# Optimization experiments

Measured on AMD Instinct MI355X. Metric: run time of the kernel, lower is better.

The kernel has to match this reference:

```python
import jax, jax.numpy as jnp
import numpy as np

N = 100000   # nodes
F = 128      # input features
H = 128      # hidden = 2*output_dim
Z = 64       # output_dim
E = 1600000  # message-passing edges
EP = 200000  # pos/neg decode edges each


def setup_inputs() -> dict:
    key = jax.random.key(0)
    ks = jax.random.split(key, 6)
    x = jax.random.normal(ks[0], (N, F), dtype=jnp.float32)
    edge_index = jax.random.randint(ks[1], (2, E), 0, N, dtype=jnp.int64)
    pos_edge = jax.random.randint(ks[2], (2, EP), 0, N, dtype=jnp.int64)
    neg_edge = jax.random.randint(ks[3], (2, EP), 0, N, dtype=jnp.int64)
    W1 = jax.random.normal(ks[4], (F, H), dtype=jnp.float32) / np.float32(np.sqrt(F))
    b1 = jnp.zeros((H,), jnp.float32)
    W2 = jax.random.normal(ks[5], (H, Z), dtype=jnp.float32) / np.float32(np.sqrt(H))
    b2 = jnp.zeros((Z,), jnp.float32)
    return dict(x=x, W1=W1, b1=b1, W2=W2, b2=b2,
                edge_index=edge_index, pos_edge=pos_edge, neg_edge=neg_edge)


def _gcn_conv(x, src, dst, norm, W, b, n):
    # x' = scatter_add_dst(norm * (x @ W)[src]) + b   (GCNConv, sym-normalized, self-loops)
    h = x @ W                         # [N, out]
    msg = h[src] * norm[:, None]      # [E+N, out] gather + scale
    out = jax.ops.segment_sum(msg, dst, num_segments=n)
    return out + b


def reference(x, W1, b1, W2, b2, edge_index, pos_edge, neg_edge):
    # add self-loops (GCNConv default)
    loop = jnp.arange(N, dtype=edge_index.dtype)
    src = jnp.concatenate([edge_index[0], loop])
    dst = jnp.concatenate([edge_index[1], loop])
    # symmetric normalization deg^-1/2[src] * deg^-1/2[dst]
    deg = jax.ops.segment_sum(jnp.ones(dst.shape, x.dtype), dst, num_segments=N)
    dinv = jnp.where(deg > 0, jax.lax.rsqrt(deg), 0.0)
    norm = dinv[src] * dinv[dst]
    # encoder: GCN -> ReLU -> GCN
    h = jax.nn.relu(_gcn_conv(x, src, dst, norm, W1, b1, N))
    latent = _gcn_conv(h, src, dst, norm, W2, b2, N)
    # decoder: edge dot products on pos+neg edges
    e = jnp.concatenate([pos_edge, neg_edge], axis=-1)  # [2, 2*EP]
    logits = jnp.sum(latent[e[0]] * latent[e[1]], axis=-1)
    return logits
```

## Files before the change

kernel.cpp:

```cpp
#include <hip/hip_runtime.h>

#define N_NODES 100000
#define F_IN    128
#define H_DIM   128
#define Z_DIM   64
#define E_EDGES 1600000
#define EP_EDGES 200000

#define BSHIFT 7
#define NBUCK  ((N_NODES + 127) >> 7)
#define CHUNK  4096
#define NCHUNK ((E_EDGES + CHUNK - 1) / CHUNK)

typedef __attribute__((ext_vector_type(8))) short short8;
typedef __attribute__((ext_vector_type(4))) float f32x4;
typedef unsigned int uint;
typedef unsigned short ushort;

__device__ __forceinline__ ushort f2bf(float f) {
    uint u = __float_as_uint(f);
    u += 0x7fffu + ((u >> 16) & 1u);
    return (ushort)(u >> 16);
}
__device__ __forceinline__ float bflo(uint u) { return __uint_as_float(u << 16); }
__device__ __forceinline__ float bfhi(uint u) { return __uint_as_float(u & 0xffff0000u); }


__global__ __launch_bounds__(256) void zero_gcur_kernel(int* __restrict__ gcur) {
    int i = blockIdx.x * 256 + threadIdx.x;
    if (i < 1024) gcur[i] = 0;
}


__global__ __launch_bounds__(256) void bhist_kernel(const int* __restrict__ dst,
                                                    int* __restrict__ ghist) {
    __shared__ int lh[NBUCK];
    for (int i = threadIdx.x; i < NBUCK; i += 256) lh[i] = 0;
    __syncthreads();
    int base = blockIdx.x * CHUNK;
    int end = min(base + CHUNK, E_EDGES);
    for (int e = base + threadIdx.x; e < end; e += 256)
        atomicAdd(&lh[dst[e] >> BSHIFT], 1);
    __syncthreads();
    for (int i = threadIdx.x; i < NBUCK; i += 256)
        if (lh[i]) atomicAdd(&ghist[i], lh[i]);
}


__global__ __launch_bounds__(1024) void bscan_kernel(int* __restrict__ gc) {
    __shared__ int s[1024];
    int t = threadIdx.x;
    int v = (t < NBUCK) ? gc[t] : 0;
    s[t] = v;
    __syncthreads();
    #pragma unroll
    for (int off = 1; off < 1024; off <<= 1) {
        int x = (t >= off) ? s[t - off] : 0;
        __syncthreads();
        s[t] += x;
        __syncthreads();
    }
    if (t < NBUCK) gc[t] = s[t] - v;
}


__global__ __launch_bounds__(256) void bscatter_kernel(const int* __restrict__ src,
                                                       const int* __restrict__ dst,
                                                       int* __restrict__ gcursor,
                                                       int* __restrict__ sorted) {
    __shared__ int lh[NBUCK];
    __shared__ int lbase[NBUCK];
    for (int i = threadIdx.x; i < NBUCK; i += 256) lh[i] = 0;
    __syncthreads();
    int base = blockIdx.x * CHUNK;
    int end = min(base + CHUNK, E_EDGES);
    for (int e = base + threadIdx.x; e < end; e += 256)
        atomicAdd(&lh[dst[e] >> BSHIFT], 1);
    __syncthreads();
    for (int i = threadIdx.x; i < NBUCK; i += 256)
        lbase[i] = lh[i] ? atomicAdd(&gcursor[i], lh[i]) : 0;
    __syncthreads();
    for (int e = base + threadIdx.x; e < end; e += 256) {
        int d = dst[e];
        int p = atomicAdd(&lbase[d >> BSHIFT], 1);
        sorted[p] = (src[e] << 7) | (d & 127);
    }
}


__global__ __launch_bounds__(256) void bucket_csr_kernel(const int* __restrict__ sorted,
                                                         const int* __restrict__ gcur,
                                                         int* __restrict__ csr,
                                                         int* __restrict__ ends,
                                                         float* __restrict__ dinv) {
    __shared__ int lcnt[128], lcur[128];
    int b = blockIdx.x, t = threadIdx.x;
    int bstart = b ? gcur[b - 1] : 0;
    int bend = gcur[b];
    if (t < 128) lcnt[t] = 0;
    __syncthreads();
    for (int i = bstart + t; i < bend; i += 256)
        atomicAdd(&lcnt[sorted[i] & 127], 1);
    __syncthreads();
    if (t < 64) {
        int c0 = lcnt[t], c1 = lcnt[t + 64];
        int s0 = c0;
        #pragma unroll
        for (int d = 1; d < 64; d <<= 1) {
            int x = __shfl_up(s0, d, 64);
            if (t >= d) s0 += x;
        }
        int tot0 = __shfl(s0, 63, 64);
        int s1 = c1;
        #pragma unroll
        for (int d = 1; d < 64; d <<= 1) {
            int x = __shfl_up(s1, d, 64);
            if (t >= d) s1 += x;
        }
        s1 += tot0;
        lcur[t] = s0 - c0;
        lcur[t + 64] = s1 - c1;
        int n0 = b * 128 + t, n1 = n0 + 64;
        if (n0 < N_NODES) { ends[n0] = bstart + s0; dinv[n0] = rsqrtf(1.0f + (float)c0); }
        if (n1 < N_NODES) { ends[n1] = bstart + s1; dinv[n1] = rsqrtf(1.0f + (float)c1); }
    }
    __syncthreads();
    for (int i = bstart + t; i < bend; i += 256) {
        int v = sorted[i];
        int p = bstart + atomicAdd(&lcur[v & 127], 1);
        csr[p] = v >> 7;
    }
}


__global__ __launch_bounds__(256) void wprep_kernel(const float* __restrict__ W1,
                                                    const float* __restrict__ W2,
                                                    ushort* __restrict__ W1T,
                                                    ushort* __restrict__ W2T) {
    int i = blockIdx.x * 256 + threadIdx.x;
    if (i < 128 * 128) {
        int n = i >> 7, k = i & 127;
        W1T[i] = f2bf(W1[k * 128 + n]);
    }
    int j = i - 128 * 128;
    if (j >= 0 && j < 64 * 128) {
        int n = j >> 7, k = j & 127;
        W2T[j] = f2bf(W2[k * 64 + n]);
    }
}


template<int NC, bool A_F32>
__global__ __launch_bounds__(256) void gemm_mfma_kernel(const void* __restrict__ Ap,
                                                        const ushort* __restrict__ BT,
                                                        const float* __restrict__ dinv,
                                                        ushort* __restrict__ C, int M) {
    constexpr int NT = NC / 16;
    __shared__ ushort Bs[4 * NT * 64 * 8];

    for (int idx = threadIdx.x; idx < 4 * NT * 64; idx += 256) {
        int l   = idx & 63;
        int nt  = (idx >> 6) % NT;
        int kc  = idx / (64 * NT);
        int m16 = l & 15, quad = l >> 4;
        ((short8*)Bs)[idx] =
            *(const short8*)(BT + ((nt * 16 + m16) * 128 + kc * 32 + quad * 8));
    }
    __syncthreads();

    int wave = threadIdx.x >> 6, lane = threadIdx.x & 63;
    int m16 = lane & 15, quad = lane >> 4;
    int row0 = (blockIdx.x * 4 + wave) * 16;
    if (row0 >= M) return;
    int arow = row0 + m16;
    if (arow >= M) arow = M - 1;

    f32x4 acc[NT];
    #pragma unroll
    for (int t = 0; t < NT; ++t) acc[t] = (f32x4){0.f, 0.f, 0.f, 0.f};

    #pragma unroll
    for (int kc = 0; kc < 4; ++kc) {
        short8 a;
        if (A_F32) {
            const float* A = (const float*)Ap;
            const float4* p = (const float4*)(A + (size_t)arow * 128 + kc * 32 + quad * 8);
            float4 x0 = p[0], x1 = p[1];
            a[0] = (short)f2bf(x0.x); a[1] = (short)f2bf(x0.y);
            a[2] = (short)f2bf(x0.z); a[3] = (short)f2bf(x0.w);
            a[4] = (short)f2bf(x1.x); a[5] = (short)f2bf(x1.y);
            a[6] = (short)f2bf(x1.z); a[7] = (short)f2bf(x1.w);
        } else {
            a = *(const short8*)((const ushort*)Ap + (size_t)arow * 128 + kc * 32 + quad * 8);
        }
        #pragma unroll
        for (int nt = 0; nt < NT; ++nt) {
            short8 b = ((const short8*)Bs)[(kc * NT + nt) * 64 + lane];
            acc[nt] = __builtin_amdgcn_mfma_f32_16x16x32_bf16(a, b, acc[nt], 0, 0, 0);
        }
    }

    #pragma unroll
    for (int r = 0; r < 4; ++r) {
        int row = row0 + quad * 4 + r;
        if (row < M) {
            float dr = dinv[row];
            #pragma unroll
            for (int nt = 0; nt < NT; ++nt)
                C[(size_t)row * NC + nt * 16 + m16] = f2bf(acc[nt][r] * dr);
        }
    }
}


__global__ __launch_bounds__(256) void gather128_kernel(const ushort* __restrict__ feat,
                                                        const float* __restrict__ bias,
                                                        const float* __restrict__ dinv,
                                                        const int* __restrict__ ends,
                                                        const int* __restrict__ csr,
                                                        ushort* __restrict__ out) {
    int wave = threadIdx.x >> 6, lane = threadIdx.x & 63;
    int half = lane >> 5, sl = lane & 31;
    int n = blockIdx.x * 4 + wave;
    const uint2* fu = (const uint2*)feat;

    float a0 = 0.f, a1 = 0.f, a2 = 0.f, a3 = 0.f;
    if (half == 0) {
        uint2 s = fu[(size_t)n * 32 + sl];
        a0 = bflo(s.x); a1 = bfhi(s.x); a2 = bflo(s.y); a3 = bfhi(s.y);
    }
    int j0 = n ? ends[n - 1] : 0, j1 = ends[n];
    int j = j0 + half;
    for (; j + 14 < j1; j += 16) {
        int s0 = csr[j],      s1 = csr[j + 2],  s2 = csr[j + 4],  s3 = csr[j + 6];
        int s4 = csr[j + 8],  s5 = csr[j + 10], s6 = csr[j + 12], s7 = csr[j + 14];
        uint2 f0 = fu[(size_t)s0 * 32 + sl];
        uint2 f1 = fu[(size_t)s1 * 32 + sl];
        uint2 f2 = fu[(size_t)s2 * 32 + sl];
        uint2 f3 = fu[(size_t)s3 * 32 + sl];
        uint2 f4 = fu[(size_t)s4 * 32 + sl];
        uint2 f5 = fu[(size_t)s5 * 32 + sl];
        uint2 f6 = fu[(size_t)s6 * 32 + sl];
        uint2 f7 = fu[(size_t)s7 * 32 + sl];
        a0 += bflo(f0.x) + bflo(f1.x) + bflo(f2.x) + bflo(f3.x)
            + bflo(f4.x) + bflo(f5.x) + bflo(f6.x) + bflo(f7.x);
        a1 += bfhi(f0.x) + bfhi(f1.x) + bfhi(f2.x) + bfhi(f3.x)
            + bfhi(f4.x) + bfhi(f5.x) + bfhi(f6.x) + bfhi(f7.x);
        a2 += bflo(f0.y) + bflo(f1.y) + bflo(f2.y) + bflo(f3.y)
            + bflo(f4.y) + bflo(f5.y) + bflo(f6.y) + bflo(f7.y);
        a3 += bfhi(f0.y) + bfhi(f1.y) + bfhi(f2.y) + bfhi(f3.y)
            + bfhi(f4.y) + bfhi(f5.y) + bfhi(f6.y) + bfhi(f7.y);
    }
    for (; j + 6 < j1; j += 8) {
        int s0 = csr[j], s1 = csr[j + 2], s2 = csr[j + 4], s3 = csr[j + 6];
        uint2 f0 = fu[(size_t)s0 * 32 + sl];
        uint2 f1 = fu[(size_t)s1 * 32 + sl];
        uint2 f2 = fu[(size_t)s2 * 32 + sl];
        uint2 f3 = fu[(size_t)s3 * 32 + sl];
        a0 += bflo(f0.x) + bflo(f1.x) + bflo(f2.x) + bflo(f3.x);
        a1 += bfhi(f0.x) + bfhi(f1.x) + bfhi(f2.x) + bfhi(f3.x);
        a2 += bflo(f0.y) + bflo(f1.y) + bflo(f2.y) + bflo(f3.y);
        a3 += bfhi(f0.y) + bfhi(f1.y) + bfhi(f2.y) + bfhi(f3.y);
    }
    for (; j < j1; j += 2) {
        uint2 f = fu[(size_t)csr[j] * 32 + sl];
        a0 += bflo(f.x); a1 += bfhi(f.x); a2 += bflo(f.y); a3 += bfhi(f.y);
    }
    a0 += __shfl_xor(a0, 32, 64);
    a1 += __shfl_xor(a1, 32, 64);
    a2 += __shfl_xor(a2, 32, 64);
    a3 += __shfl_xor(a3, 32, 64);
    if (half == 0) {
        float dn = dinv[n];
        float r0 = fmaxf(bias[sl * 4 + 0] + dn * a0, 0.f);
        float r1 = fmaxf(bias[sl * 4 + 1] + dn * a1, 0.f);
        float r2 = fmaxf(bias[sl * 4 + 2] + dn * a2, 0.f);
        float r3 = fmaxf(bias[sl * 4 + 3] + dn * a3, 0.f);
        uint2 o;
        o.x = (uint)f2bf(r0) | ((uint)f2bf(r1) << 16);
        o.y = (uint)f2bf(r2) | ((uint)f2bf(r3) << 16);
        ((uint2*)out)[(size_t)n * 32 + sl] = o;
    }
}


__global__ __launch_bounds__(256) void gather64_kernel(const ushort* __restrict__ feat,
                                                       const float* __restrict__ bias,
                                                       const float* __restrict__ dinv,
                                                       const int* __restrict__ ends,
                                                       const int* __restrict__ csr,
                                                       ushort* __restrict__ outB) {
    int wave = threadIdx.x >> 6, lane = threadIdx.x & 63;
    int half = lane >> 5, sl = lane & 31;
    int n = blockIdx.x * 4 + wave;
    const uint* fu = (const uint*)feat;

    float a0 = 0.f, a1 = 0.f;
    if (half == 0) {
        uint s = fu[(size_t)n * 32 + sl];
        a0 = bflo(s); a1 = bfhi(s);
    }
    int j0 = n ? ends[n - 1] : 0, j1 = ends[n];
    int j = j0 + half;
    for (; j + 14 < j1; j += 16) {
        int s0 = csr[j],      s1 = csr[j + 2],  s2 = csr[j + 4],  s3 = csr[j + 6];
        int s4 = csr[j + 8],  s5 = csr[j + 10], s6 = csr[j + 12], s7 = csr[j + 14];
        uint f0 = fu[(size_t)s0 * 32 + sl];
        uint f1 = fu[(size_t)s1 * 32 + sl];
        uint f2 = fu[(size_t)s2 * 32 + sl];
        uint f3 = fu[(size_t)s3 * 32 + sl];
        uint f4 = fu[(size_t)s4 * 32 + sl];
        uint f5 = fu[(size_t)s5 * 32 + sl];
        uint f6 = fu[(size_t)s6 * 32 + sl];
        uint f7 = fu[(size_t)s7 * 32 + sl];
        a0 += bflo(f0) + bflo(f1) + bflo(f2) + bflo(f3)
            + bflo(f4) + bflo(f5) + bflo(f6) + bflo(f7);
        a1 += bfhi(f0) + bfhi(f1) + bfhi(f2) + bfhi(f3)
            + bfhi(f4) + bfhi(f5) + bfhi(f6) + bfhi(f7);
    }
    for (; j + 6 < j1; j += 8) {
        int s0 = csr[j], s1 = csr[j + 2], s2 = csr[j + 4], s3 = csr[j + 6];
        uint f0 = fu[(size_t)s0 * 32 + sl];
        uint f1 = fu[(size_t)s1 * 32 + sl];
        uint f2 = fu[(size_t)s2 * 32 + sl];
        uint f3 = fu[(size_t)s3 * 32 + sl];
        a0 += bflo(f0) + bflo(f1) + bflo(f2) + bflo(f3);
        a1 += bfhi(f0) + bfhi(f1) + bfhi(f2) + bfhi(f3);
    }
    for (; j < j1; j += 2) {
        uint f = fu[(size_t)csr[j] * 32 + sl];
        a0 += bflo(f); a1 += bfhi(f);
    }
    a0 += __shfl_xor(a0, 32, 64);
    a1 += __shfl_xor(a1, 32, 64);
    if (half == 0) {
        float dn = dinv[n];
        float o0 = bias[sl * 2]     + dn * a0;
        float o1 = bias[sl * 2 + 1] + dn * a1;
        ((uint*)outB)[(size_t)n * 32 + sl] = (uint)f2bf(o0) | ((uint)f2bf(o1) << 16);
    }
}


__global__ __launch_bounds__(256) void decode_kernel(const ushort* __restrict__ latentB,
                                                     const int* __restrict__ pos,
                                                     const int* __restrict__ neg,
                                                     float* __restrict__ out) {
    int gwave = (blockIdx.x * 256 + threadIdx.x) >> 6;
    int lane = threadIdx.x & 63;
    int half = lane >> 5, sl = lane & 31;
    const uint* L = (const uint*)latentB;
    int e0 = gwave * 8 + half * 4;
    if (e0 >= 2 * EP_EDGES) return;

    int ia[4], ib[4];
    #pragma unroll
    for (int u = 0; u < 4; ++u) {
        int edge = e0 + u;
        if (edge < EP_EDGES) {
            ia[u] = pos[edge];
            ib[u] = pos[EP_EDGES + edge];
        } else {
            int e2 = edge - EP_EDGES;
            ia[u] = neg[e2];
            ib[u] = neg[EP_EDGES + e2];
        }
    }
    uint la[4], lb[4];
    #pragma unroll
    for (int u = 0; u < 4; ++u) {
        la[u] = L[(size_t)ia[u] * 32 + sl];
        lb[u] = L[(size_t)ib[u] * 32 + sl];
    }
    float v[4];
    #pragma unroll
    for (int u = 0; u < 4; ++u)
        v[u] = bflo(la[u]) * bflo(lb[u]) + bfhi(la[u]) * bfhi(lb[u]);
    #pragma unroll
    for (int u = 0; u < 4; ++u) {
        float s = v[u];
        #pragma unroll
        for (int off = 16; off > 0; off >>= 1) s += __shfl_down(s, off, 64);
        if (sl == 0) out[e0 + u] = s;
    }
}


extern "C" void kernel_launch(void* const* d_in, const int* in_sizes, int n_in,
                              void* d_out, int out_size, void* d_ws, size_t ws_size,
                              hipStream_t stream) {
    const float* x  = (const float*)d_in[0];
    const float* W1 = (const float*)d_in[1];
    const float* b1 = (const float*)d_in[2];
    const float* W2 = (const float*)d_in[3];
    const float* b2 = (const float*)d_in[4];
    const int* edge_index = (const int*)d_in[5];
    const int* pos = (const int*)d_in[6];
    const int* neg = (const int*)d_in[7];
    float* out = (float*)d_out;

    const int* src = edge_index;
    const int* dst = edge_index + E_EDGES;

    float*  dinv   = (float*)d_ws;
    int*    ends   = (int*)(dinv + N_NODES);
    int*    gcur   = ends + N_NODES;
    int*    sorted = gcur + 1024;
    int*    csr    = sorted + E_EDGES;
    ushort* W1T    = (ushort*)(csr + E_EDGES);
    ushort* W2T    = W1T + 128 * 128;
    ushort* bufH   = W2T + 64 * 128;
    ushort* bufR   = bufH + (size_t)N_NODES * 128;

    zero_gcur_kernel<<<4, 256, 0, stream>>>(gcur);
    bhist_kernel<<<NCHUNK, 256, 0, stream>>>(dst, gcur);
    bscan_kernel<<<1, 1024, 0, stream>>>(gcur);
    bscatter_kernel<<<NCHUNK, 256, 0, stream>>>(src, dst, gcur, sorted);
    bucket_csr_kernel<<<NBUCK, 256, 0, stream>>>(sorted, gcur, csr, ends, dinv);

    wprep_kernel<<<96, 256, 0, stream>>>(W1, W2, W1T, W2T);

    const int GEMM_GRID = (N_NODES + 63) / 64;

    gemm_mfma_kernel<128, true><<<GEMM_GRID, 256, 0, stream>>>(x, W1T, dinv, bufH, N_NODES);

    gather128_kernel<<<N_NODES / 4, 256, 0, stream>>>(bufH, b1, dinv, ends, csr, bufR);

    gemm_mfma_kernel<64, false><<<GEMM_GRID, 256, 0, stream>>>(bufR, W2T, dinv, bufH, N_NODES);

    ushort* latentB = bufR;
    gather64_kernel<<<N_NODES / 4, 256, 0, stream>>>(bufH, b2, dinv, ends, csr, latentB);

    decode_kernel<<<(2 * EP_EDGES) / 32, 256, 0, stream>>>(latentB, pos, neg, out);
}
```

Before: 322.6 us.

## Replace scatter-time global atomics with per-chunk offset table and per-wave local counts

The histogram kernel now writes each chunk's per-bucket counts to a table, and a new column-wise scan kernel turns those counts into deterministic per-chunk base offsets. The scatter pass then no longer recomputes the local histogram or does global atomics. It only loads its precomputed bases. The CSR build splits its LDS counters per wave to reduce atomic contention, and the weight-prep kernel is merged with zeroing the counters to save a launch. In exchange it adds an extra scan kernel and a table of NCHUNK×NBUCK ints read and written through global memory.

```diff
diff --git a/kernel.cpp b/kernel.cpp
--- a/kernel.cpp
+++ b/kernel.cpp
@@ -26,14 +26,28 @@
 __device__ __forceinline__ float bfhi(uint u) { return __uint_as_float(u & 0xffff0000u); }
 
 
-__global__ __launch_bounds__(256) void zero_gcur_kernel(int* __restrict__ gcur) {
+__global__ __launch_bounds__(256) void wprep_kernel(const float* __restrict__ W1,
+                                                    const float* __restrict__ W2,
+                                                    ushort* __restrict__ W1T,
+                                                    ushort* __restrict__ W2T,
+                                                    int* __restrict__ gcur) {
     int i = blockIdx.x * 256 + threadIdx.x;
     if (i < 1024) gcur[i] = 0;
+    if (i < 128 * 128) {
+        int n = i >> 7, k = i & 127;
+        W1T[i] = f2bf(W1[k * 128 + n]);
+    }
+    int j = i - 128 * 128;
+    if (j >= 0 && j < 64 * 128) {
+        int n = j >> 7, k = j & 127;
+        W2T[j] = f2bf(W2[k * 64 + n]);
+    }
 }
 
 
 __global__ __launch_bounds__(256) void bhist_kernel(const int* __restrict__ dst,
-                                                    int* __restrict__ ghist) {
+                                                    int* __restrict__ gcur,
+                                                    int* __restrict__ tbl) {
     __shared__ int lh[NBUCK];
     for (int i = threadIdx.x; i < NBUCK; i += 256) lh[i] = 0;
     __syncthreads();
@@ -42,8 +56,12 @@
     for (int e = base + threadIdx.x; e < end; e += 256)
         atomicAdd(&lh[dst[e] >> BSHIFT], 1);
     __syncthreads();
-    for (int i = threadIdx.x; i < NBUCK; i += 256)
-        if (lh[i]) atomicAdd(&ghist[i], lh[i]);
+    int* trow = tbl + (size_t)blockIdx.x * NBUCK;
+    for (int i = threadIdx.x; i < NBUCK; i += 256) {
+        int c = lh[i];
+        trow[i] = c;
+        if (c) atomicAdd(&gcur[i], c);
+    }
 }
 
 
@@ -64,22 +82,36 @@
 }
 
 
+__global__ __launch_bounds__(512) void chunk_scan_kernel(int* __restrict__ tbl,
+                                                         const int* __restrict__ gcur) {
+    __shared__ int s[512];
+    int b = blockIdx.x, t = threadIdx.x;
+    int v = (t < NCHUNK) ? tbl[(size_t)t * NBUCK + b] : 0;
+    s[t] = v;
+    __syncthreads();
+    #pragma unroll
+    for (int off = 1; off < 512; off <<= 1) {
+        int x = (t >= off) ? s[t - off] : 0;
+        __syncthreads();
+        s[t] += x;
+        __syncthreads();
+    }
+    if (t < NCHUNK)
+        tbl[(size_t)t * NBUCK + b] = gcur[b] + (s[t] - v);
+}
+
+
 __global__ __launch_bounds__(256) void bscatter_kernel(const int* __restrict__ src,
                                                        const int* __restrict__ dst,
-                                                       int* __restrict__ gcursor,
+                                                       const int* __restrict__ tbl,
                                                        int* __restrict__ sorted) {
-    __shared__ int lh[NBUCK];
     __shared__ int lbase[NBUCK];
-    for (int i = threadIdx.x; i < NBUCK; i += 256) lh[i] = 0;
-    __syncthreads();
-    int base = blockIdx.x * CHUNK;
+    int c = blockIdx.x;
+    const int* trow = tbl + (size_t)c * NBUCK;
+    for (int i = threadIdx.x; i < NBUCK; i += 256) lbase[i] = trow[i];
+    __syncthreads();
+    int base = c * CHUNK;
     int end = min(base + CHUNK, E_EDGES);
-    for (int e = base + threadIdx.x; e < end; e += 256)
-        atomicAdd(&lh[dst[e] >> BSHIFT], 1);
-    __syncthreads();
-    for (int i = threadIdx.x; i < NBUCK; i += 256)
-        lbase[i] = lh[i] ? atomicAdd(&gcursor[i], lh[i]) : 0;
-    __syncthreads();
     for (int e = base + threadIdx.x; e < end; e += 256) {
         int d = dst[e];
         int p = atomicAdd(&lbase[d >> BSHIFT], 1);
@@ -93,17 +125,22 @@
                                                          int* __restrict__ csr,
                                                          int* __restrict__ ends,
                                                          float* __restrict__ dinv) {
-    __shared__ int lcnt[128], lcur[128];
+    __shared__ int lcnt[4][128], lcur[4][128];
     int b = blockIdx.x, t = threadIdx.x;
-    int bstart = b ? gcur[b - 1] : 0;
-    int bend = gcur[b];
-    if (t < 128) lcnt[t] = 0;
+    int wave = t >> 6, lane = t & 63;
+    int bstart = gcur[b];
+    int bend = (b + 1 < NBUCK) ? gcur[b + 1] : E_EDGES;
+    if (t < 128) { lcnt[0][t] = 0; lcnt[1][t] = 0; }
+    else { int u = t - 128; lcnt[2][u] = 0; lcnt[3][u] = 0; }
     __syncthreads();
     for (int i = bstart + t; i < bend; i += 256)
-        atomicAdd(&lcnt[sorted[i] & 127], 1);
+        atomicAdd(&lcnt[wave][sorted[i] & 127], 1);
     __syncthreads();
     if (t < 64) {
-        int c0 = lcnt[t], c1 = lcnt[t + 64];
+        int w0a = lcnt[0][t], w1a = lcnt[1][t], w2a = lcnt[2][t], w3a = lcnt[3][t];
+        int w0b = lcnt[0][t + 64], w1b = lcnt[1][t + 64], w2b = lcnt[2][t + 64], w3b = lcnt[3][t + 64];
+        int c0 = w0a + w1a + w2a + w3a;
+        int c1 = w0b + w1b + w2b + w3b;
         int s0 = c0;
         #pragma unroll
         for (int d = 1; d < 64; d <<= 1) {
@@ -118,8 +155,16 @@
             if (t >= d) s1 += x;
         }
         s1 += tot0;
-        lcur[t] = s0 - c0;
-        lcur[t + 64] = s1 - c1;
+        int basea = bstart + s0 - c0;
+        int baseb = bstart + s1 - c1;
+        lcur[0][t] = basea;
+        lcur[1][t] = basea + w0a;
+        lcur[2][t] = basea + w0a + w1a;
+        lcur[3][t] = basea + w0a + w1a + w2a;
+        lcur[0][t + 64] = baseb;
+        lcur[1][t + 64] = baseb + w0b;
+        lcur[2][t + 64] = baseb + w0b + w1b;
+        lcur[3][t + 64] = baseb + w0b + w1b + w2b;
         int n0 = b * 128 + t, n1 = n0 + 64;
         if (n0 < N_NODES) { ends[n0] = bstart + s0; dinv[n0] = rsqrtf(1.0f + (float)c0); }
         if (n1 < N_NODES) { ends[n1] = bstart + s1; dinv[n1] = rsqrtf(1.0f + (float)c1); }
@@ -127,25 +172,8 @@
     __syncthreads();
     for (int i = bstart + t; i < bend; i += 256) {
         int v = sorted[i];
-        int p = bstart + atomicAdd(&lcur[v & 127], 1);
+        int p = atomicAdd(&lcur[wave][v & 127], 1);
         csr[p] = v >> 7;
-    }
-}
-
-
-__global__ __launch_bounds__(256) void wprep_kernel(const float* __restrict__ W1,
-                                                    const float* __restrict__ W2,
-                                                    ushort* __restrict__ W1T,
-                                                    ushort* __restrict__ W2T) {
-    int i = blockIdx.x * 256 + threadIdx.x;
-    if (i < 128 * 128) {
-        int n = i >> 7, k = i & 127;
-        W1T[i] = f2bf(W1[k * 128 + n]);
-    }
-    int j = i - 128 * 128;
-    if (j >= 0 && j < 64 * 128) {
-        int n = j >> 7, k = j & 127;
-        W2T[j] = f2bf(W2[k * 64 + n]);
     }
 }
 
@@ -405,20 +433,21 @@
     float*  dinv   = (float*)d_ws;
     int*    ends   = (int*)(dinv + N_NODES);
     int*    gcur   = ends + N_NODES;
-    int*    sorted = gcur + 1024;
+    int*    tbl    = gcur + 1024;
+    int*    sorted = tbl + NCHUNK * NBUCK;
     int*    csr    = sorted + E_EDGES;
     ushort* W1T    = (ushort*)(csr + E_EDGES);
     ushort* W2T    = W1T + 128 * 128;
     ushort* bufH   = W2T + 64 * 128;
     ushort* bufR   = bufH + (size_t)N_NODES * 128;
 
-    zero_gcur_kernel<<<4, 256, 0, stream>>>(gcur);
-    bhist_kernel<<<NCHUNK, 256, 0, stream>>>(dst, gcur);
+    wprep_kernel<<<96, 256, 0, stream>>>(W1, W2, W1T, W2T, gcur);
+
+    bhist_kernel<<<NCHUNK, 256, 0, stream>>>(dst, gcur, tbl);
     bscan_kernel<<<1, 1024, 0, stream>>>(gcur);
-    bscatter_kernel<<<NCHUNK, 256, 0, stream>>>(src, dst, gcur, sorted);
+    chunk_scan_kernel<<<NBUCK, 512, 0, stream>>>(tbl, gcur);
+    bscatter_kernel<<<NCHUNK, 256, 0, stream>>>(src, dst, tbl, sorted);
     bucket_csr_kernel<<<NBUCK, 256, 0, stream>>>(sorted, gcur, csr, ends, dinv);
-
-    wprep_kernel<<<96, 256, 0, stream>>>(W1, W2, W1T, W2T);
 
     const int GEMM_GRID = (N_NODES + 63) / 64;
 
```

Measured after the change: 349.1 us. 8.2% more time.
